# Optimization experiments

Hardware: AMD Instinct MI355X
Metric: run time of the kernel (lower is better)

## Reference

```python
import jax, jax.numpy as jnp
import numpy as np

B, S, FIN, FOUT = 16, 50000, 16, 16
E, T = 8000000, 64


def setup_inputs() -> dict:
    key = jax.random.key(0)
    k1, k2, k3, k4, k5 = jax.random.split(key, 5)
    x = jax.random.normal(k1, (B, S, FIN), dtype=jnp.float32)
    weight = jax.random.normal(k2, (T,), dtype=jnp.float32)
    rows = jax.random.randint(k3, (E,), 0, S * FOUT, dtype=jnp.int32)
    cols = jax.random.randint(k4, (E,), 0, S * FIN, dtype=jnp.int32)
    edge_type = jax.random.randint(k5, (E,), 0, T, dtype=jnp.int32)
    return {"x": x, "weight": weight, "rows": rows, "cols": cols,
            "edge_type": edge_type, "out_features": FOUT}


def reference(x, weight, rows, cols, edge_type, out_features):
    # x: [B, S, Fin] -> flatten(1).t(): [S*Fin, B]
    b, s, fin = x.shape
    inp = x.reshape(b, s * fin).T                      # [S*Fin, B]
    w = weight[edge_type]                              # gather per-edge weight, [E]
    msgs = w[:, None] * inp[cols]                      # [E, B] gathered source signals
    out = jax.ops.segment_sum(msgs, rows, num_segments=s * out_features)  # sparse mm
    return out.T.reshape(b, s, out_features)           # [B, S, Fout]
```

## Files before the change

### kernel.cpp

```cpp
#include <hip/hip_runtime.h>

#define BNUM 16
#define NCOL 800000
#define NROW 800000
#define RPB  1024
#define NBIN 782
#define HB   1024
#define PR   8192
#define PT   512
#define CAPF 11264

#define WG_ADD(p, v) __hip_atomic_fetch_add((p), (v), __ATOMIC_RELAXED, __HIP_MEMORY_SCOPE_WORKGROUP)

__device__ __forceinline__ unsigned short f2bf(float f) {
    unsigned u = __float_as_uint(f);
    unsigned r = (u + 0x7fffu + ((u >> 16) & 1u)) >> 16;
    return (unsigned short)r;
}
__device__ __forceinline__ float bf2f(unsigned short h) {
    return __uint_as_float(((unsigned)h) << 16);
}

template <int BITS>
__device__ __forceinline__ void brank(unsigned key, bool v, int lane,
                                      int& rank, int& gsz) {
    unsigned long long vm = __ballot(v);
    unsigned long long eq = ~0ull;
#pragma unroll
    for (int b = 0; b < BITS; ++b) {
        unsigned long long bb = __ballot((key >> b) & 1u);
        eq &= ((key >> b) & 1u) ? bb : ~bb;
    }
    eq &= vm;
    rank = __popcll(eq & ((1ull << lane) - 1ull));
    gsz  = __popcll(eq);
}

__global__ __launch_bounds__(256) void k_transpose_x(const float* __restrict__ x,
                                                     unsigned* __restrict__ xT) {
    int c = blockIdx.x * 256 + threadIdx.x;
    if (c >= NCOL) return;
    unsigned p[8];
#pragma unroll
    for (int b = 0; b < 8; ++b) {
        float lo = x[(size_t)(2 * b)     * NCOL + c];
        float hi = x[(size_t)(2 * b + 1) * NCOL + c];
        p[b] = (unsigned)f2bf(lo) | ((unsigned)f2bf(hi) << 16);
    }
    uint4* dst = reinterpret_cast<uint4*>(xT + (size_t)c * 8);
    dst[0] = make_uint4(p[0], p[1], p[2], p[3]);
    dst[1] = make_uint4(p[4], p[5], p[6], p[7]);
}

__global__ __launch_bounds__(1024) void k_init(unsigned* __restrict__ cursor) {
    int t = threadIdx.x;
    cursor[t] = (unsigned)t * CAPF;
}

__global__ __launch_bounds__(PT) void k_place(const int* __restrict__ rows,
                                              const int* __restrict__ cols,
                                              const int* __restrict__ et,
                                              unsigned* __restrict__ cursor,
                                              unsigned* __restrict__ recA,
                                              unsigned short* __restrict__ recB,
                                              int E) {
    __shared__ unsigned cnt[HB];
    __shared__ unsigned lofs[HB];
    __shared__ unsigned gbase[HB];
    __shared__ unsigned srtA[PR];
    __shared__ unsigned srtR[PR];
    __shared__ unsigned wsum[8];

    int t  = threadIdx.x;
    int c0 = blockIdx.x * PR;
    int c1 = min(E, c0 + PR);
    int tot = c1 - c0;

    for (int i = t; i < HB; i += PT) cnt[i] = 0u;
    __syncthreads();

    unsigned er[16], ec[16];
#pragma unroll
    for (int k = 0; k < 16; ++k) {
        int e = c0 + k * PT + t;
        if (e < c1) {
            int r  = __builtin_nontemporal_load(rows + e);
            int c  = __builtin_nontemporal_load(cols + e);
            int ty = __builtin_nontemporal_load(et + e);
            er[k] = (unsigned)r;
            ec[k] = (unsigned)c | ((unsigned)ty << 20);
        } else {
            er[k] = 0xFFFFFFFFu;
            ec[k] = 0u;
        }
    }
#pragma unroll
    for (int k = 0; k < 16; ++k)
        if (er[k] != 0xFFFFFFFFu) WG_ADD(&cnt[er[k] >> 10], 1u);
    __syncthreads();

    {
        unsigned a0 = cnt[2 * t];
        unsigned a1 = cnt[2 * t + 1];
        unsigned ts = a0 + a1;
        unsigned incl = ts;
        for (int off = 1; off < 64; off <<= 1) {
            unsigned n = __shfl_up(incl, off, 64);
            if ((t & 63) >= off) incl += n;
        }
        if ((t & 63) == 63) wsum[t >> 6] = incl;
        __syncthreads();
        unsigned pre = 0;
        for (int k2 = 0; k2 < (t >> 6); ++k2) pre += wsum[k2];
        unsigned ex = pre + incl - ts;
        lofs[2 * t]     = ex;
        lofs[2 * t + 1] = ex + a0;
    }
    __syncthreads();

    for (int i = t; i < HB; i += PT) {
        unsigned c = cnt[i];
        gbase[i] = c ? atomicAdd(&cursor[i], c) : 0u;
    }
    __syncthreads();
    for (int i = t; i < HB; i += PT) cnt[i] = 0u;
    __syncthreads();

#pragma unroll
    for (int k = 0; k < 16; ++k) {
        if (er[k] == 0xFFFFFFFFu) continue;
        unsigned b  = er[k] >> 10;
        unsigned lr = er[k] & 1023u;
        unsigned rk = WG_ADD(&cnt[b], 1u);
        unsigned j  = lofs[b] + rk;
        srtA[j] = ec[k];
        srtR[j] = (b << 10) | lr;
    }
    __syncthreads();

    for (int j = t; j < tot; j += PT) {
        unsigned rr = srtR[j];
        unsigned b  = rr >> 10;
        unsigned dst = gbase[b] + ((unsigned)j - lofs[b]);
        if (dst < (b + 1u) * CAPF) {
            recA[dst] = srtA[j];
            recB[dst] = (unsigned short)(rr & 1023u);
        }
    }
}

__device__ __forceinline__ void fma8(float* a, float wt, uint4 v, int base) {
    a[base + 0] += wt * bf2f((unsigned short)(v.x & 0xffffu));
    a[base + 1] += wt * bf2f((unsigned short)(v.x >> 16));
    a[base + 2] += wt * bf2f((unsigned short)(v.y & 0xffffu));
    a[base + 3] += wt * bf2f((unsigned short)(v.y >> 16));
    a[base + 4] += wt * bf2f((unsigned short)(v.z & 0xffffu));
    a[base + 5] += wt * bf2f((unsigned short)(v.z >> 16));
    a[base + 6] += wt * bf2f((unsigned short)(v.w & 0xffffu));
    a[base + 7] += wt * bf2f((unsigned short)(v.w >> 16));
}

__global__ __launch_bounds__(1024) void k_pull(const unsigned* __restrict__ cursor,
                                               const unsigned* __restrict__ recA,
                                               const unsigned short* __restrict__ recB,
                                               const float* __restrict__ wt_tab,
                                               const unsigned* __restrict__ xT,
                                               float* __restrict__ out) {
    __shared__ unsigned short h16[16][RPB];
    __shared__ unsigned srt[CAPF];
    __shared__ unsigned short ptr_[RPB + 1];
    __shared__ unsigned wsum[16];

    int tid = threadIdx.x, lane = tid & 63, wv = tid >> 6;
    int bin = blockIdx.x;
    unsigned sbeg = (unsigned)bin * CAPF;
    int n  = min((int)(cursor[bin] - sbeg), CAPF);
    int nr = (n + 1023) >> 10;

    unsigned* hw = (unsigned*)h16;
    for (int i = tid; i < 16 * RPB / 2; i += 1024) hw[i] = 0u;
    __syncthreads();

    for (int c = 0; c < nr; ++c) {
        int idx = c * 1024 + tid;
        bool v = idx < n;
        unsigned key = 0u;
        if (v) key = recB[sbeg + idx] & (RPB - 1u);
        int rank, gsz;
        brank<10>(key, v, lane, rank, gsz);
        if (v && rank == 0)
            h16[wv][key] = (unsigned short)(h16[wv][key] + (unsigned)gsz);
    }
    __syncthreads();

    {
        unsigned t0 = 0;
#pragma unroll
        for (int ww = 0; ww < 16; ++ww) {
            unsigned a = h16[ww][tid]; h16[ww][tid] = (unsigned short)t0; t0 += a;
        }
        unsigned incl = t0;
        for (int off = 1; off < 64; off <<= 1) {
            unsigned m = __shfl_up(incl, off, 64);
            if ((tid & 63) >= off) incl += m;
        }
        if ((tid & 63) == 63) wsum[tid >> 6] = incl;
        __syncthreads();
        unsigned pre = 0;
        for (int k = 0; k < (tid >> 6); ++k) pre += wsum[k];
        unsigned ex = pre + incl - t0;
        ptr_[tid] = (unsigned short)ex;
        if (tid == 1023) ptr_[RPB] = (unsigned short)n;
#pragma unroll
        for (int ww = 0; ww < 16; ++ww)
            h16[ww][tid] = (unsigned short)(h16[ww][tid] + ex);
    }
    __syncthreads();

    for (int c = 0; c < nr; ++c) {
        int idx = c * 1024 + tid;
        bool v = idx < n;
        unsigned key = 0u, pay = 0u;
        if (v) {
            key = recB[sbeg + idx] & (RPB - 1u);
            pay = recA[sbeg + idx];
        }
        int rank, gsz;
        brank<10>(key, v, lane, rank, gsz);
        unsigned cur = h16[wv][key];
        if (v && rank == 0)
            h16[wv][key] = (unsigned short)(cur + (unsigned)gsz);
        if (v) srt[cur + (unsigned)rank] = pay;
    }
    __syncthreads();

    int r = tid;
    float a[16];
#pragma unroll
    for (int k = 0; k < 16; ++k) a[k] = 0.f;
    {
        int p0 = (int)ptr_[r];
        int p1 = (int)ptr_[r + 1];
        int len  = p1 - p0;
        int lcap = min(len, 32);

        unsigned m0 = 0, m1 = 0, m2 = 0, m3 = 0, m4 = 0, m5 = 0, m6 = 0, m7 = 0;
        for (int i = 0; i < lcap; ++i) {
            unsigned oct = (srt[p0 + i] >> 17) & 7u;
            unsigned bit = 1u << i;
            m0 |= (oct == 0u) ? bit : 0u;
            m1 |= (oct == 1u) ? bit : 0u;
            m2 |= (oct == 2u) ? bit : 0u;
            m3 |= (oct == 3u) ? bit : 0u;
            m4 |= (oct == 4u) ? bit : 0u;
            m5 |= (oct == 5u) ? bit : 0u;
            m6 |= (oct == 6u) ? bit : 0u;
            m7 |= (oct == 7u) ? bit : 0u;
        }

#define GATHER_MASK(MQ)                                                       \
        {                                                                     \
            unsigned mask = (MQ);                                             \
            while (mask) {                                                    \
                int i = __ffs(mask) - 1;                                      \
                mask &= mask - 1u;                                            \
                unsigned u = srt[p0 + i];                                     \
                const uint4* qp = reinterpret_cast<const uint4*>(             \
                    xT + (size_t)(u & 0xFFFFFu) * 8);                         \
                uint4 lo = qp[0], hi = qp[1];                                 \
                float wt = wt_tab[u >> 20];                                   \
                fma8(a, wt, lo, 0);                                           \
                fma8(a, wt, hi, 8);                                           \
            }                                                                 \
        }
        GATHER_MASK(m0) GATHER_MASK(m1) GATHER_MASK(m2) GATHER_MASK(m3)
        GATHER_MASK(m4) GATHER_MASK(m5) GATHER_MASK(m6) GATHER_MASK(m7)
#undef GATHER_MASK

        for (int p = p0 + 32; p < p1; ++p) {
            unsigned u = srt[p];
            const uint4* qp = reinterpret_cast<const uint4*>(
                xT + (size_t)(u & 0xFFFFFu) * 8);
            uint4 lo = qp[0], hi = qp[1];
            float wt = wt_tab[u >> 20];
            fma8(a, wt, lo, 0);
            fma8(a, wt, hi, 8);
        }
    }
    int gr = bin * RPB + r;
    if (gr < NROW) {
#pragma unroll
        for (int k = 0; k < 16; ++k)
            __builtin_nontemporal_store(a[k], out + (size_t)k * NROW + gr);
    }
}


__global__ __launch_bounds__(256) void k_scatter(const int* __restrict__ rows,
                                                 const int* __restrict__ cols,
                                                 const int* __restrict__ et,
                                                 const float* __restrict__ w,
                                                 const unsigned* __restrict__ xT,
                                                 unsigned short* __restrict__ outT,
                                                 int E) {
    long long tid = (long long)blockIdx.x * 256 + threadIdx.x;
    long long e = tid >> 3;
    if (e >= E) return;
    int j = (int)(tid & 7);
    int r = __builtin_nontemporal_load(rows + e);
    int c = __builtin_nontemporal_load(cols + e);
    int t = __builtin_nontemporal_load(et + e);
    float wt = w[t];
    unsigned px = xT[(size_t)c * 8 + j];
    float x0 = bf2f((unsigned short)(px & 0xffffu));
    float x1 = bf2f((unsigned short)(px >> 16));
    unsigned short b0 = f2bf(wt * x0);
    unsigned short b1 = f2bf(wt * x1);
    unsigned data = (unsigned)b0 | ((unsigned)b1 << 16);
    unsigned short* dst = outT + ((size_t)r * 16 + 2 * j);
    asm volatile("global_atomic_pk_add_bf16 %0, %1, off"
                 :: "v"(dst), "v"(data) : "memory");
}

__global__ __launch_bounds__(256) void k_transpose_out(const unsigned* __restrict__ outT,
                                                       float* __restrict__ out) {
    int r = blockIdx.x * 256 + threadIdx.x;
    if (r >= NROW) return;
    const uint4* src = reinterpret_cast<const uint4*>(outT + (size_t)r * 8);
    uint4 v0 = src[0], v1 = src[1];
    unsigned p[8] = {v0.x, v0.y, v0.z, v0.w, v1.x, v1.y, v1.z, v1.w};
#pragma unroll
    for (int b = 0; b < 8; ++b) {
        out[(size_t)(2 * b)     * NROW + r] = bf2f((unsigned short)(p[b] & 0xffffu));
        out[(size_t)(2 * b + 1) * NROW + r] = bf2f((unsigned short)(p[b] >> 16));
    }
}

extern "C" void kernel_launch(void* const* d_in, const int* in_sizes, int n_in,
                              void* d_out, int out_size, void* d_ws, size_t ws_size,
                              hipStream_t stream) {
    const float* x    = (const float*)d_in[0];
    const float* w    = (const float*)d_in[1];
    const int*   rows = (const int*)d_in[2];
    const int*   cols = (const int*)d_in[3];
    const int*   et   = (const int*)d_in[4];
    const int    E    = in_sizes[2];

    float* out = (float*)d_out;

    size_t xT_b    = (size_t)NCOL * 8 * 4;
    size_t slabN   = (size_t)NBIN * CAPF;
    size_t rA_off  = xT_b;
    size_t rB_off  = rA_off + slabN * 4;
    size_t aux_off = (rB_off + slabN * 2 + 255) & ~(size_t)255;
    size_t needed  = aux_off + 1024 * 4;

    unsigned* xT = (unsigned*)d_ws;

    if (ws_size >= needed) {
        unsigned*       recA   = (unsigned*)((char*)d_ws + rA_off);
        unsigned short* recB   = (unsigned short*)((char*)d_ws + rB_off);
        unsigned*       cursor = (unsigned*)((char*)d_ws + aux_off);

        k_init<<<1, 1024, 0, stream>>>(cursor);
        k_transpose_x<<<NCOL / 256, 256, 0, stream>>>(x, xT);

        int pblocks = (E + PR - 1) / PR;
        k_place<<<pblocks, PT, 0, stream>>>(rows, cols, et, cursor, recA, recB, E);
        k_pull<<<NBIN, 1024, 0, stream>>>(cursor, recA, recB, w, xT, out);
    } else {
        unsigned short* outT = (unsigned short*)d_ws;
        unsigned*       xT2  = (unsigned*)((char*)d_ws + (size_t)NROW * BNUM * 2);

        hipMemsetAsync(outT, 0, (size_t)NROW * BNUM * 2, stream);
        k_transpose_x<<<NCOL / 256, 256, 0, stream>>>(x, xT2);

        long long total = (long long)E * 8;
        int blocks = (int)((total + 255) / 256);
        k_scatter<<<blocks, 256, 0, stream>>>(rows, cols, et, w, xT2, outT, E);
        k_transpose_out<<<NROW / 256, 256, 0, stream>>>((const unsigned*)outT, out);
    }
}
```

Before: 232.6 us.

## Fuse x transpose into placement kernel and software-pipeline gather loads

The x-to-bf16 transpose now runs inside the edge-placement kernel as extra trailing blocks, which removes one kernel launch and lets the transpose overlap with edge bucketing. In the pull kernel's gather loop, the load for the next edge is issued before the FMAs for the previous edge, so memory latency is hidden behind arithmetic. The pipelining holds one extra set of loaded values in registers, raising register pressure, and the transpose blocks now share the placement kernel's large shared-memory footprint, which may limit how many of them fit per CU.

```diff
diff --git a/kernel.cpp b/kernel.cpp
--- a/kernel.cpp
+++ b/kernel.cpp
@@ -57,13 +57,15 @@
     cursor[t] = (unsigned)t * CAPF;
 }
 
-__global__ __launch_bounds__(PT) void k_place(const int* __restrict__ rows,
+__global__ __launch_bounds__(PT) void k_fused(const int* __restrict__ rows,
                                               const int* __restrict__ cols,
                                               const int* __restrict__ et,
                                               unsigned* __restrict__ cursor,
                                               unsigned* __restrict__ recA,
                                               unsigned short* __restrict__ recB,
-                                              int E) {
+                                              int E, int pblocks,
+                                              const float* __restrict__ x,
+                                              unsigned* __restrict__ xT) {
     __shared__ unsigned cnt[HB];
     __shared__ unsigned lofs[HB];
     __shared__ unsigned gbase[HB];
@@ -71,7 +73,25 @@
     __shared__ unsigned srtR[PR];
     __shared__ unsigned wsum[8];
 
-    int t  = threadIdx.x;
+    int t = threadIdx.x;
+
+    if ((int)blockIdx.x >= pblocks) {
+        int c = ((int)blockIdx.x - pblocks) * PT + t;
+        if (c < NCOL) {
+            unsigned p[8];
+#pragma unroll
+            for (int b = 0; b < 8; ++b) {
+                float lo = x[(size_t)(2 * b)     * NCOL + c];
+                float hi = x[(size_t)(2 * b + 1) * NCOL + c];
+                p[b] = (unsigned)f2bf(lo) | ((unsigned)f2bf(hi) << 16);
+            }
+            uint4* dst = reinterpret_cast<uint4*>(xT + (size_t)c * 8);
+            dst[0] = make_uint4(p[0], p[1], p[2], p[3]);
+            dst[1] = make_uint4(p[4], p[5], p[6], p[7]);
+        }
+        return;
+    }
+
     int c0 = blockIdx.x * PR;
     int c1 = min(E, c0 + PR);
     int tot = c1 - c0;
@@ -258,33 +278,48 @@
             m7 |= (oct == 7u) ? bit : 0u;
         }
 
-#define GATHER_MASK(MQ)                                                       \
+        unsigned pu = 0u;
+        uint4 plo = make_uint4(0, 0, 0, 0), phi = plo;
+        bool have = false;
+
+#define STEP_MASK(MQ)                                                         \
         {                                                                     \
             unsigned mask = (MQ);                                             \
             while (mask) {                                                    \
                 int i = __ffs(mask) - 1;                                      \
                 mask &= mask - 1u;                                            \
-                unsigned u = srt[p0 + i];                                     \
+                unsigned nu = srt[p0 + i];                                    \
                 const uint4* qp = reinterpret_cast<const uint4*>(             \
-                    xT + (size_t)(u & 0xFFFFFu) * 8);                         \
-                uint4 lo = qp[0], hi = qp[1];                                 \
-                float wt = wt_tab[u >> 20];                                   \
-                fma8(a, wt, lo, 0);                                           \
-                fma8(a, wt, hi, 8);                                           \
+                    xT + (size_t)(nu & 0xFFFFFu) * 8);                        \
+                uint4 nlo = qp[0], nhi = qp[1];                               \
+                if (have) {                                                   \
+                    float wt = wt_tab[pu >> 20];                              \
+                    fma8(a, wt, plo, 0);                                      \
+                    fma8(a, wt, phi, 8);                                      \
+                }                                                             \
+                pu = nu; plo = nlo; phi = nhi; have = true;                   \
             }                                                                 \
         }
-        GATHER_MASK(m0) GATHER_MASK(m1) GATHER_MASK(m2) GATHER_MASK(m3)
-        GATHER_MASK(m4) GATHER_MASK(m5) GATHER_MASK(m6) GATHER_MASK(m7)
-#undef GATHER_MASK
+        STEP_MASK(m0) STEP_MASK(m1) STEP_MASK(m2) STEP_MASK(m3)
+        STEP_MASK(m4) STEP_MASK(m5) STEP_MASK(m6) STEP_MASK(m7)
+#undef STEP_MASK
 
         for (int p = p0 + 32; p < p1; ++p) {
-            unsigned u = srt[p];
+            unsigned nu = srt[p];
             const uint4* qp = reinterpret_cast<const uint4*>(
-                xT + (size_t)(u & 0xFFFFFu) * 8);
-            uint4 lo = qp[0], hi = qp[1];
-            float wt = wt_tab[u >> 20];
-            fma8(a, wt, lo, 0);
-            fma8(a, wt, hi, 8);
+                xT + (size_t)(nu & 0xFFFFFu) * 8);
+            uint4 nlo = qp[0], nhi = qp[1];
+            if (have) {
+                float wt = wt_tab[pu >> 20];
+                fma8(a, wt, plo, 0);
+                fma8(a, wt, phi, 8);
+            }
+            pu = nu; plo = nlo; phi = nhi; have = true;
+        }
+        if (have) {
+            float wt = wt_tab[pu >> 20];
+            fma8(a, wt, plo, 0);
+            fma8(a, wt, phi, 8);
         }
     }
     int gr = bin * RPB + r;
@@ -363,21 +398,23 @@
         unsigned*       cursor = (unsigned*)((char*)d_ws + aux_off);
 
         k_init<<<1, 1024, 0, stream>>>(cursor);
-        k_transpose_x<<<NCOL / 256, 256, 0, stream>>>(x, xT);
 
         int pblocks = (E + PR - 1) / PR;
-        k_place<<<pblocks, PT, 0, stream>>>(rows, cols, et, cursor, recA, recB, E);
+        int tblocks = (NCOL + PT - 1) / PT;
+        k_fused<<<pblocks + tblocks, PT, 0, stream>>>(rows, cols, et, cursor,
+                                                      recA, recB, E, pblocks,
+                                                      x, xT);
         k_pull<<<NBIN, 1024, 0, stream>>>(cursor, recA, recB, w, xT, out);
     } else {
         unsigned short* outT = (unsigned short*)d_ws;
         unsigned*       xT2  = (unsigned*)((char*)d_ws + (size_t)NROW * BNUM * 2);
 
         hipMemsetAsync(outT, 0, (size_t)NROW * BNUM * 2, stream);
-        k_transpose_x<<<NCOL / 256, 256, 0, stream>>>(x, xT2);
+        k_transpose_x<<<(NCOL + 255) / 256, 256, 0, stream>>>(x, xT2);
 
         long long total = (long long)E * 8;
         int blocks = (int)((total + 255) / 256);
         k_scatter<<<blocks, 256, 0, stream>>>(rows, cols, et, w, xT2, outT, E);
-        k_transpose_out<<<NROW / 256, 256, 0, stream>>>((const unsigned*)outT, out);
-    }
-}
+        k_transpose_out<<<(NROW + 255) / 256, 256, 0, stream>>>((const unsigned*)outT, out);
+    }
+}
```

Result: slower. 268.0 us (+15.2%).
